# Kernel optimization log

Measured on AMD Instinct MI355X. Metric: run time of the kernel, lower is better.

## Reference

```python
import jax, jax.numpy as jnp
import numpy as np
from jax import lax

T, B, D, H, C = 2048, 64, 128, 256, 5

def setup_inputs() -> dict:
    key = jax.random.key(0)
    k = jax.random.split(key, 7)
    s = 1.0 / np.sqrt(H)  # pytorch nn.RNN init scale
    return {
        "inputs": jax.random.normal(k[0], (T, B, D), dtype=jnp.float32),
        "W_ih": jax.random.uniform(k[1], (H, D), jnp.float32, -s, s),
        "W_hh": jax.random.uniform(k[2], (H, H), jnp.float32, -s, s),
        "b_ih": jax.random.uniform(k[3], (H,), jnp.float32, -s, s),
        "b_hh": jax.random.uniform(k[4], (H,), jnp.float32, -s, s),
        "W_fc": jax.random.uniform(k[5], (C, H), jnp.float32, -s, s),
        "b_fc": jax.random.uniform(k[6], (C,), jnp.float32, -s, s),
    }

def reference(inputs, W_ih, W_hh, b_ih, b_hh, W_fc, b_fc):
    # Precompute input projections for all timesteps: (T, B, H)
    x_proj = jnp.einsum('tbd,hd->tbh', inputs, W_ih) + b_ih + b_hh

    def step(h, xp):
        # h_t = tanh(W_ih x_t + b_ih + W_hh h_{t-1} + b_hh)
        h_new = jnp.tanh(xp + h @ W_hh.T)
        return h_new, None  # per-step outputs unused by the module head

    h0 = jnp.zeros((inputs.shape[1], W_hh.shape[0]), dtype=inputs.dtype)
    h_last, _ = lax.scan(step, h0, x_proj)

    logits = h_last @ W_fc.T + b_fc  # (B, 5)
    return jax.nn.log_softmax(logits, axis=1)
```

## Files before the change

### kernel.cpp

```cpp
#include <hip/hip_runtime.h>


#define T_DIM 2048
#define B_DIM 64
#define D_DIM 128
#define H_DIM 256
#define C_DIM 5

using floatx4 = __attribute__((ext_vector_type(4))) float;
using shortx8 = __attribute__((ext_vector_type(8))) short;

#define W_SCALE 2032.0f
#define H_SCALE 127.0f
#define INV_SCALE (1.0f / (2032.0f * 127.0f))

__device__ __forceinline__ short f2bf(float f) {
  unsigned int u = __float_as_uint(f);
  unsigned int r = (u + 0x7FFFu + ((u >> 16) & 1u)) >> 16;
  return (short)r;
}

__device__ __forceinline__ int sdot4(unsigned int a, unsigned int b, int c) {
#if __has_builtin(__builtin_amdgcn_sdot4)
  return __builtin_amdgcn_sdot4((int)a, (int)b, c, false);
#else
  int r = c;
  #pragma unroll
  for (int k = 0; k < 4; ++k)
    r += (int)(signed char)(a >> (8 * k)) * (int)(signed char)(b >> (8 * k));
  return r;
#endif
}

template<int CTRL>
__device__ __forceinline__ int dpp_movi(int x) {
  return __builtin_amdgcn_update_dpp(0, x, CTRL, 0xF, 0xF, true);
}

__device__ __forceinline__ void barrier_lds_only() {
  asm volatile("s_waitcnt lgkmcnt(0)\n\ts_barrier" ::: "memory");
}

#define TS_PER_BLOCK 2
__global__ __launch_bounds__(256) void xp_kernel(
    const float* __restrict__ x,
    const float* __restrict__ W_ih,
    const float* __restrict__ b_ih,
    const float* __restrict__ b_hh,
    _Float16* __restrict__ xp,
    int cnt)
{
  __shared__ __align__(16) short wlds[32768];
  const int tid = threadIdx.x;
  {
    const int group = tid >> 2;
    const int sub = tid & 3;
    const int kf = group & 3;
    const int k0 = kf * 32 + sub * 8;
    #pragma unroll
    for (int i = 0; i < 16; ++i) {
      const int n = (group >> 2) * 16 + i;
      const float* src = W_ih + n * D_DIM + k0;
      float4 p0 = *(const float4*)(src);
      float4 p1 = *(const float4*)(src + 4);
      shortx8 v;
      v[0]=f2bf(p0.x); v[1]=f2bf(p0.y); v[2]=f2bf(p0.z); v[3]=f2bf(p0.w);
      v[4]=f2bf(p1.x); v[5]=f2bf(p1.y); v[6]=f2bf(p1.z); v[7]=f2bf(p1.w);
      *(shortx8*)&wlds[(group * 64 + sub * 16 + i) * 8] = v;
    }
  }
  __syncthreads();

  const int wv   = tid >> 6;
  const int lane = tid & 63;
  const int col  = lane & 15;
  const int quad = lane >> 4;

  float bias[16];
  #pragma unroll
  for (int nt = 0; nt < 16; ++nt)
    bias[nt] = b_ih[nt * 16 + col] + b_hh[nt * 16 + col];

  for (int tl = 0; tl < TS_PER_BLOCK; ++tl) {
    const int t = blockIdx.x * TS_PER_BLOCK + tl;
    if (t >= cnt) break;
    const long m0 = (long)t * 64 + wv * 16;

    shortx8 af[4];
    const float* arow = x + (m0 + col) * D_DIM + quad * 8;
    #pragma unroll
    for (int kf = 0; kf < 4; ++kf) {
      float4 p0 = *(const float4*)(arow + kf * 32);
      float4 p1 = *(const float4*)(arow + kf * 32 + 4);
      shortx8 v;
      v[0]=f2bf(p0.x); v[1]=f2bf(p0.y); v[2]=f2bf(p0.z); v[3]=f2bf(p0.w);
      v[4]=f2bf(p1.x); v[5]=f2bf(p1.y); v[6]=f2bf(p1.z); v[7]=f2bf(p1.w);
      af[kf] = v;
    }

    #pragma unroll
    for (int nt = 0; nt < 16; ++nt) {
      floatx4 acc = {0.f, 0.f, 0.f, 0.f};
      #pragma unroll
      for (int kf = 0; kf < 4; ++kf) {
        shortx8 bfrag = *(const shortx8*)&wlds[((nt * 4 + kf) * 64 + lane) * 8];
        acc = __builtin_amdgcn_mfma_f32_16x16x32_bf16(af[kf], bfrag, acc, 0, 0, 0);
      }
      const int n = nt * 16 + col;
      #pragma unroll
      for (int r = 0; r < 4; ++r) {
        const long m = m0 + quad * 4 + r;
        xp[m * H_DIM + n] = (_Float16)(acc[r] + bias[nt]);
      }
    }
  }
}

__global__ __launch_bounds__(256)
__attribute__((amdgpu_waves_per_eu(1, 1)))
void scan_kernel(
    const _Float16* __restrict__ xp,
    const float* __restrict__ W_hh,
    const float* __restrict__ W_fc,
    const float* __restrict__ b_fc,
    float* __restrict__ h_state,
    float* __restrict__ out,
    int cnt, int first, int last)
{
  __shared__ __align__(16) signed char hbuf[2][256];
  __shared__ float hfin[H_DIM];
  __shared__ float scratch[192];
  const int b   = blockIdx.x;
  const int tid = threadIdx.x;
  const int g   = tid >> 2;
  const int c   = tid & 3;

  unsigned int wq[4][16];
  const float* wbase = W_hh + (g * 4) * H_DIM + c * 64;
  #pragma unroll
  for (int r = 0; r < 4; ++r)
    #pragma unroll
    for (int i = 0; i < 16; ++i) {
      float4 f = *(const float4*)(wbase + r * H_DIM + i * 4);
      unsigned int q0 = (unsigned int)(int)rintf(f.x * W_SCALE) & 0xFFu;
      unsigned int q1 = (unsigned int)(int)rintf(f.y * W_SCALE) & 0xFFu;
      unsigned int q2 = (unsigned int)(int)rintf(f.z * W_SCALE) & 0xFFu;
      unsigned int q3 = (unsigned int)(int)rintf(f.w * W_SCALE) & 0xFFu;
      wq[r][i] = q0 | (q1 << 8) | (q2 << 16) | (q3 << 24);
    }
  #pragma unroll
  for (int r = 0; r < 4; ++r)
    #pragma unroll
    for (int i = 0; i < 16; ++i)
      asm volatile("" : "+v"(wq[r][i]));

  const int row_w = tid;
  {
    float h0 = first ? 0.f : h_state[b * H_DIM + row_w];
    hbuf[0][row_w] = (signed char)(int)rintf(h0 * H_SCALE);
  }
  __syncthreads();

  const size_t BH = (size_t)B_DIM * H_DIM;
  const _Float16* xpp = xp + (size_t)b * H_DIM + row_w;
  float hnlast = 0.f;

  auto step_body = [&](int bufsel, _Float16 xin) -> void {
    const signed char* hb = hbuf[bufsel] + c * 64;
    uint4 u0 = *(const uint4*)(hb);
    uint4 u1 = *(const uint4*)(hb + 16);
    uint4 u2 = *(const uint4*)(hb + 32);
    uint4 u3 = *(const uint4*)(hb + 48);
    const unsigned int hv[16] = {u0.x, u0.y, u0.z, u0.w, u1.x, u1.y, u1.z, u1.w,
                                 u2.x, u2.y, u2.z, u2.w, u3.x, u3.y, u3.z, u3.w};
    int a0 = 0, a1 = 0, a2 = 0, a3 = 0;
    #pragma unroll
    for (int i = 0; i < 16; ++i) {
      a0 = sdot4(wq[0][i], hv[i], a0);
      a1 = sdot4(wq[1][i], hv[i], a1);
      a2 = sdot4(wq[2][i], hv[i], a2);
      a3 = sdot4(wq[3][i], hv[i], a3);
    }
    int k01 = (c & 1) ? a1 : a0;
    int s01 = (c & 1) ? a0 : a1;
    int m0  = k01 + dpp_movi<0xB1>(s01);
    int k23 = (c & 1) ? a3 : a2;
    int s23 = (c & 1) ? a2 : a3;
    int m1  = k23 + dpp_movi<0xB1>(s23);
    int kk = (c & 2) ? m1 : m0;
    int sn = (c & 2) ? m0 : m1;
    int vi = kk + dpp_movi<0x4E>(sn);

    float p = (float)vi * INV_SCALE + (float)xin;
    float e   = __expf(2.f * p);
    float hqf = 127.f - __fdividef(254.f, e + 1.f);
    hnlast = hqf;
    hbuf[bufsel ^ 1][row_w] = (signed char)(int)rintf(hqf);
    barrier_lds_only();
  };

  if ((cnt & 1) == 0 && cnt >= 2) {
    const _Float16* p = xpp;
    _Float16 x0 = p[0];
    _Float16 x1 = p[BH];
    int s = 0;
    for (; s + 2 < cnt; s += 2) {
      step_body(0, x0); x0 = p[2 * BH];
      step_body(1, x1); x1 = p[3 * BH];
      p += 2 * BH;
    }
    step_body(0, x0);
    step_body(1, x1);
  } else {
    for (int s = 0; s < cnt; ++s)
      step_body(s & 1, xpp[(size_t)s * BH]);
  }

  {
    const float hT = hnlast * (1.0f / 127.0f);
    h_state[b * H_DIM + row_w] = hT;
    hfin[row_w] = hT;
  }

  if (last) {
    __syncthreads();
    if (tid < 160) {
      const int c5 = tid >> 5, i = tid & 31;
      float pp = 0.f;
      #pragma unroll
      for (int jj = 0; jj < 8; ++jj) {
        const int j = i * 8 + jj;
        pp += W_fc[c5 * H_DIM + j] * hfin[j];
      }
      scratch[tid] = pp;
    }
    __syncthreads();
    if (tid < C_DIM) {
      float l = b_fc[tid];
      for (int i = 0; i < 32; ++i) l += scratch[tid * 32 + i];
      scratch[160 + tid] = l;
    }
    __syncthreads();
    if (tid == 0) {
      float mx = scratch[160];
      for (int i = 1; i < C_DIM; ++i) mx = fmaxf(mx, scratch[160 + i]);
      float se = 0.f;
      for (int i = 0; i < C_DIM; ++i) se += __expf(scratch[160 + i] - mx);
      const float lse = mx + __logf(se);
      for (int i = 0; i < C_DIM; ++i) out[b * C_DIM + i] = scratch[160 + i] - lse;
    }
  }
}

extern "C" void kernel_launch(void* const* d_in, const int* in_sizes, int n_in,
                              void* d_out, int out_size, void* d_ws, size_t ws_size,
                              hipStream_t stream) {
  (void)in_sizes; (void)n_in; (void)out_size;
  const float* x    = (const float*)d_in[0];
  const float* W_ih = (const float*)d_in[1];
  const float* W_hh = (const float*)d_in[2];
  const float* b_ih = (const float*)d_in[3];
  const float* b_hh = (const float*)d_in[4];
  const float* W_fc = (const float*)d_in[5];
  const float* b_fc = (const float*)d_in[6];
  float* out = (float*)d_out;

  char* ws = (char*)d_ws;
  float* h_state = (float*)ws;
  _Float16* xp = (_Float16*)(ws + 65536);
  const size_t avail = ws_size > 65536 ? ws_size - 65536 : 0;
  long Tc = (long)(avail / ((size_t)B_DIM * H_DIM * sizeof(_Float16)));
  if (Tc > T_DIM) Tc = T_DIM;
  if (Tc < 1) Tc = 1;

  for (long t0 = 0; t0 < T_DIM; t0 += Tc) {
    const long cnt = (T_DIM - t0 < Tc) ? (T_DIM - t0) : Tc;
    const unsigned xpb = (unsigned)((cnt + TS_PER_BLOCK - 1) / TS_PER_BLOCK);
    xp_kernel<<<dim3(xpb), dim3(256), 0, stream>>>(
        x + t0 * B_DIM * D_DIM, W_ih, b_ih, b_hh, xp, (int)cnt);
    scan_kernel<<<dim3(B_DIM), dim3(256), 0, stream>>>(
        xp, W_hh, W_fc, b_fc, h_state, out,
        (int)cnt, t0 == 0 ? 1 : 0, (t0 + cnt == T_DIM) ? 1 : 0);
  }
}
```

Measured before the change: 737.7 us.

## Overlap next-chunk input projection with recurrent scan via fused double-buffered kernel

Runs the sequential scan in chunks. Each launch is a fused kernel whose first 64 blocks run the recurrence for the current chunk while the remaining blocks compute the input projection for the next chunk into a second buffer. This hides the projection work behind the latency-bound scan and removes the serial xp-then-scan dependency between launches. The tanh step is also rewritten with exp2, a hardware reciprocal and a magic-number int8 rounding. The dot-product accumulators are split into two chains, and the hidden state is carried between chunks as int8 instead of float. The trade-offs are more launches with an unbalanced grid, and contention between the scan blocks and the projection blocks for memory bandwidth.

```diff
diff --git a/kernel.cpp b/kernel.cpp
--- a/kernel.cpp
+++ b/kernel.cpp
@@ -13,6 +13,9 @@
 #define W_SCALE 2032.0f
 #define H_SCALE 127.0f
 #define INV_SCALE (1.0f / (2032.0f * 127.0f))
+#define TWO_LOG2E 2.8853900817779268f
+#define K_EXP (TWO_LOG2E * INV_SCALE)
+#define MAGIC 12582912.0f
 
 __device__ __forceinline__ short f2bf(float f) {
   unsigned int u = __float_as_uint(f);
@@ -37,20 +40,35 @@
   return __builtin_amdgcn_update_dpp(0, x, CTRL, 0xF, 0xF, true);
 }
 
+__device__ __forceinline__ float fast_exp2(float x) {
+#if __has_builtin(__builtin_amdgcn_exp2f)
+  return __builtin_amdgcn_exp2f(x);
+#else
+  return __exp2f(x);
+#endif
+}
+
+__device__ __forceinline__ float fast_rcp(float x) {
+#if __has_builtin(__builtin_amdgcn_rcpf)
+  return __builtin_amdgcn_rcpf(x);
+#else
+  return __fdividef(1.0f, x);
+#endif
+}
+
 __device__ __forceinline__ void barrier_lds_only() {
   asm volatile("s_waitcnt lgkmcnt(0)\n\ts_barrier" ::: "memory");
 }
 
-#define TS_PER_BLOCK 2
-__global__ __launch_bounds__(256) void xp_kernel(
+__device__ __forceinline__ void xp_body(
     const float* __restrict__ x,
     const float* __restrict__ W_ih,
     const float* __restrict__ b_ih,
     const float* __restrict__ b_hh,
     _Float16* __restrict__ xp,
-    int cnt)
+    int cnt, int t0, int tstride, short* wlds)
 {
-  __shared__ __align__(16) short wlds[32768];
+  if (cnt <= 0) return;
   const int tid = threadIdx.x;
   {
     const int group = tid >> 2;
@@ -81,9 +99,7 @@
   for (int nt = 0; nt < 16; ++nt)
     bias[nt] = b_ih[nt * 16 + col] + b_hh[nt * 16 + col];
 
-  for (int tl = 0; tl < TS_PER_BLOCK; ++tl) {
-    const int t = blockIdx.x * TS_PER_BLOCK + tl;
-    if (t >= cnt) break;
+  for (int t = t0; t < cnt; t += tstride) {
     const long m0 = (long)t * 64 + wv * 16;
 
     shortx8 af[4];
@@ -116,20 +132,43 @@
   }
 }
 
+__global__ __launch_bounds__(256) void xp_kernel(
+    const float* __restrict__ x, const float* __restrict__ W_ih,
+    const float* __restrict__ b_ih, const float* __restrict__ b_hh,
+    _Float16* __restrict__ xp, int cnt)
+{
+  __shared__ __align__(16) short wlds[32768];
+  xp_body(x, W_ih, b_ih, b_hh, xp, cnt, blockIdx.x, gridDim.x, wlds);
+}
+
 __global__ __launch_bounds__(256)
 __attribute__((amdgpu_waves_per_eu(1, 1)))
-void scan_kernel(
+void fused_kernel(
     const _Float16* __restrict__ xp,
     const float* __restrict__ W_hh,
     const float* __restrict__ W_fc,
     const float* __restrict__ b_fc,
-    float* __restrict__ h_state,
+    signed char* __restrict__ h8,
     float* __restrict__ out,
-    int cnt, int first, int last)
+    int cnt, int first, int last,
+    const float* __restrict__ x_next,
+    const float* __restrict__ W_ih,
+    const float* __restrict__ b_ih,
+    const float* __restrict__ b_hh,
+    _Float16* __restrict__ xp_next,
+    int next_cnt)
 {
+  __shared__ __align__(16) short wlds[32768];
   __shared__ __align__(16) signed char hbuf[2][256];
   __shared__ float hfin[H_DIM];
   __shared__ float scratch[192];
+
+  if (blockIdx.x >= 64) {
+    xp_body(x_next, W_ih, b_ih, b_hh, xp_next, next_cnt,
+            (int)blockIdx.x - 64, (int)gridDim.x - 64, wlds);
+    return;
+  }
+
   const int b   = blockIdx.x;
   const int tid = threadIdx.x;
   const int g   = tid >> 2;
@@ -155,10 +194,7 @@
       asm volatile("" : "+v"(wq[r][i]));
 
   const int row_w = tid;
-  {
-    float h0 = first ? 0.f : h_state[b * H_DIM + row_w];
-    hbuf[0][row_w] = (signed char)(int)rintf(h0 * H_SCALE);
-  }
+  hbuf[0][row_w] = first ? (signed char)0 : h8[b * H_DIM + row_w];
   __syncthreads();
 
   const size_t BH = (size_t)B_DIM * H_DIM;
@@ -166,6 +202,7 @@
   float hnlast = 0.f;
 
   auto step_body = [&](int bufsel, _Float16 xin) -> void {
+    float xin2 = (float)xin * TWO_LOG2E;
     const signed char* hb = hbuf[bufsel] + c * 64;
     uint4 u0 = *(const uint4*)(hb);
     uint4 u1 = *(const uint4*)(hb + 16);
@@ -173,14 +210,23 @@
     uint4 u3 = *(const uint4*)(hb + 48);
     const unsigned int hv[16] = {u0.x, u0.y, u0.z, u0.w, u1.x, u1.y, u1.z, u1.w,
                                  u2.x, u2.y, u2.z, u2.w, u3.x, u3.y, u3.z, u3.w};
-    int a0 = 0, a1 = 0, a2 = 0, a3 = 0;
-    #pragma unroll
-    for (int i = 0; i < 16; ++i) {
-      a0 = sdot4(wq[0][i], hv[i], a0);
-      a1 = sdot4(wq[1][i], hv[i], a1);
-      a2 = sdot4(wq[2][i], hv[i], a2);
-      a3 = sdot4(wq[3][i], hv[i], a3);
-    }
+    int a0l = 0, a1l = 0, a2l = 0, a3l = 0;
+    int a0h = 0, a1h = 0, a2h = 0, a3h = 0;
+    #pragma unroll
+    for (int i = 0; i < 8; ++i) {
+      a0l = sdot4(wq[0][i], hv[i], a0l);
+      a1l = sdot4(wq[1][i], hv[i], a1l);
+      a2l = sdot4(wq[2][i], hv[i], a2l);
+      a3l = sdot4(wq[3][i], hv[i], a3l);
+    }
+    #pragma unroll
+    for (int i = 8; i < 16; ++i) {
+      a0h = sdot4(wq[0][i], hv[i], a0h);
+      a1h = sdot4(wq[1][i], hv[i], a1h);
+      a2h = sdot4(wq[2][i], hv[i], a2h);
+      a3h = sdot4(wq[3][i], hv[i], a3h);
+    }
+    int a0 = a0l + a0h, a1 = a1l + a1h, a2 = a2l + a2h, a3 = a3l + a3h;
     int k01 = (c & 1) ? a1 : a0;
     int s01 = (c & 1) ? a0 : a1;
     int m0  = k01 + dpp_movi<0xB1>(s01);
@@ -191,11 +237,12 @@
     int sn = (c & 2) ? m0 : m1;
     int vi = kk + dpp_movi<0x4E>(sn);
 
-    float p = (float)vi * INV_SCALE + (float)xin;
-    float e   = __expf(2.f * p);
-    float hqf = 127.f - __fdividef(254.f, e + 1.f);
-    hnlast = hqf;
-    hbuf[bufsel ^ 1][row_w] = (signed char)(int)rintf(hqf);
+    float arg = __builtin_fmaf((float)vi, K_EXP, xin2);
+    float e   = fast_exp2(arg);
+    float r   = fast_rcp(e + 1.0f);
+    hnlast    = __builtin_fmaf(-254.0f, r, 127.0f);
+    float qb  = __builtin_fmaf(-254.0f, r, MAGIC + 127.0f);
+    hbuf[bufsel ^ 1][row_w] = (signed char)__float_as_int(qb);
     barrier_lds_only();
   };
 
@@ -203,8 +250,7 @@
     const _Float16* p = xpp;
     _Float16 x0 = p[0];
     _Float16 x1 = p[BH];
-    int s = 0;
-    for (; s + 2 < cnt; s += 2) {
+    for (int s = 0; s + 2 < cnt; s += 2) {
       step_body(0, x0); x0 = p[2 * BH];
       step_body(1, x1); x1 = p[3 * BH];
       p += 2 * BH;
@@ -216,13 +262,10 @@
       step_body(s & 1, xpp[(size_t)s * BH]);
   }
 
-  {
-    const float hT = hnlast * (1.0f / 127.0f);
-    h_state[b * H_DIM + row_w] = hT;
-    hfin[row_w] = hT;
-  }
+  h8[b * H_DIM + row_w] = hbuf[cnt & 1][row_w];
 
   if (last) {
+    hfin[row_w] = hnlast * (1.0f / 127.0f);
     __syncthreads();
     if (tid < 160) {
       const int c5 = tid >> 5, i = tid & 31;
@@ -266,20 +309,53 @@
   float* out = (float*)d_out;
 
   char* ws = (char*)d_ws;
-  float* h_state = (float*)ws;
-  _Float16* xp = (_Float16*)(ws + 65536);
+  signed char* h8 = (signed char*)ws;
+  _Float16* bufA = (_Float16*)(ws + 65536);
+  const size_t step_bytes = (size_t)B_DIM * H_DIM * sizeof(_Float16);
   const size_t avail = ws_size > 65536 ? ws_size - 65536 : 0;
-  long Tc = (long)(avail / ((size_t)B_DIM * H_DIM * sizeof(_Float16)));
-  if (Tc > T_DIM) Tc = T_DIM;
-  if (Tc < 1) Tc = 1;
-
-  for (long t0 = 0; t0 < T_DIM; t0 += Tc) {
-    const long cnt = (T_DIM - t0 < Tc) ? (T_DIM - t0) : Tc;
-    const unsigned xpb = (unsigned)((cnt + TS_PER_BLOCK - 1) / TS_PER_BLOCK);
-    xp_kernel<<<dim3(xpb), dim3(256), 0, stream>>>(
-        x + t0 * B_DIM * D_DIM, W_ih, b_ih, b_hh, xp, (int)cnt);
-    scan_kernel<<<dim3(B_DIM), dim3(256), 0, stream>>>(
-        xp, W_hh, W_fc, b_fc, h_state, out,
-        (int)cnt, t0 == 0 ? 1 : 0, (t0 + cnt == T_DIM) ? 1 : 0);
-  }
-}
+  const long cap2 = (long)(avail / (2 * step_bytes));
+
+  if (cap2 >= 64) {
+    long CAP = cap2 < 512 ? cap2 : 512;
+    _Float16* bufB = bufA + (size_t)CAP * B_DIM * H_DIM;
+    long bnd[64];
+    bnd[0] = 0;
+    long c0 = 256; if (c0 > CAP) c0 = CAP; if (c0 > T_DIM) c0 = T_DIM;
+    bnd[1] = c0;
+    int nc = 1;
+    while (bnd[nc] < T_DIM && nc < 62) {
+      long nx = bnd[nc] + CAP; if (nx > T_DIM) nx = T_DIM;
+      bnd[nc + 1] = nx; ++nc;
+    }
+    {
+      const unsigned gb = (unsigned)(c0 < 512 ? c0 : 512);
+      xp_kernel<<<dim3(gb), dim3(256), 0, stream>>>(x, W_ih, b_ih, b_hh, bufA, (int)c0);
+    }
+    for (int k = 0; k < nc; ++k) {
+      _Float16* src = (k & 1) ? bufB : bufA;
+      _Float16* dst = (k & 1) ? bufA : bufB;
+      const long s0 = bnd[k], s1 = bnd[k + 1];
+      const int has_next = (k + 1 < nc) ? 1 : 0;
+      const long n0 = has_next ? bnd[k + 1] : 0;
+      const long n1 = has_next ? bnd[k + 2] : 0;
+      fused_kernel<<<dim3(256), dim3(256), 0, stream>>>(
+          src, W_hh, W_fc, b_fc, h8, out,
+          (int)(s1 - s0), k == 0 ? 1 : 0, (k == nc - 1) ? 1 : 0,
+          x + n0 * B_DIM * D_DIM, W_ih, b_ih, b_hh, dst, (int)(n1 - n0));
+    }
+  } else {
+    long Tc = (long)(avail / step_bytes);
+    if (Tc > T_DIM) Tc = T_DIM;
+    if (Tc < 1) Tc = 1;
+    for (long t0 = 0; t0 < T_DIM; t0 += Tc) {
+      const long cnt = (T_DIM - t0 < Tc) ? (T_DIM - t0) : Tc;
+      const unsigned gb = (unsigned)(cnt < 512 ? cnt : 512);
+      xp_kernel<<<dim3(gb), dim3(256), 0, stream>>>(
+          x + t0 * B_DIM * D_DIM, W_ih, b_ih, b_hh, bufA, (int)cnt);
+      fused_kernel<<<dim3(64), dim3(256), 0, stream>>>(
+          bufA, W_hh, W_fc, b_fc, h8, out,
+          (int)cnt, t0 == 0 ? 1 : 0, (t0 + cnt == T_DIM) ? 1 : 0,
+          x, W_ih, b_ih, b_hh, bufA, 0);
+    }
+  }
+}
```

New measurement: 731.2 us. No clear change (-0.9%).
